# Kernel optimization log

Measured on AMD Instinct MI355X. Metric: run time of the kernel, lower is better.

The kernel has to match this reference:

```python
import jax, jax.numpy as jnp
import numpy as np
import math

B, S, N, D, H = 4, 64, 256, 512, 8
DEPTH = D // H

def setup_inputs() -> dict:
    key = jax.random.key(0)
    ks = jax.random.split(key, 9)
    scale = 1.0 / math.sqrt(D)
    return {
        "x": jax.random.normal(ks[0], (B, S, N, D), dtype=jnp.float32),
        "Wq": jax.random.normal(ks[1], (D, D), dtype=jnp.float32) * scale,
        "bq": jax.random.normal(ks[2], (D,), dtype=jnp.float32) * 0.01,
        "Wk": jax.random.normal(ks[3], (D, D), dtype=jnp.float32) * scale,
        "bk": jax.random.normal(ks[4], (D,), dtype=jnp.float32) * 0.01,
        "Wv": jax.random.normal(ks[5], (D, D), dtype=jnp.float32) * scale,
        "bv": jax.random.normal(ks[6], (D,), dtype=jnp.float32) * 0.01,
        "Wo": jax.random.normal(ks[7], (D, D), dtype=jnp.float32) * scale,
        "bo": jax.random.normal(ks[8], (D,), dtype=jnp.float32) * 0.01,
    }

def _split_heads(t):
    # (B, S, M, D) -> (B, H, S, M, depth); matches split_head.forward (4D path)
    # followed by the att_dim==2 permute(0, 2, 1, 3, 4) in cross_attention.
    b, s, m, _ = t.shape
    return t.reshape(b, s, m, H, DEPTH).transpose(0, 3, 1, 2, 4)

def reference(x, Wq, bq, Wk, bk, Wv, bv, Wo, bo):
    b, s, n, d = x.shape
    # att_dim == 2: query is the cls token along the joint/patch axis.
    q = _split_heads(x[:, :, 0:1, :] @ Wq + bq)   # (B, H, S, 1, depth)
    k = _split_heads(x @ Wk + bk)                  # (B, H, S, N, depth)
    v = _split_heads(x @ Wv + bv)                  # (B, H, S, N, depth)
    # scaled dot product attention (mask is None in cross_attention)
    logits = jnp.einsum('bhsqd,bhskd->bhsqk', q, k) / math.sqrt(DEPTH)
    attn = jax.nn.softmax(logits, axis=-1)         # (B, H, S, 1, N)
    ctx = jnp.einsum('bhsqk,bhskd->bhsqd', attn, v)  # (B, H, S, 1, depth)
    # permute(0, 2, 3, 1, 4) then reshape (B, S, 1, D)
    concat = ctx.transpose(0, 2, 3, 1, 4).reshape(b, s, 1, d)
    return concat @ Wo + bo
```

## Files before the change

### kernel.cpp

```cpp
#include <hip/hip_runtime.h>
#include <stdint.h>
#include <math.h>


#define NT 16

__global__ __launch_bounds__(1024, 4) void fused_kernel(
    const float* __restrict__ x,
    const float* __restrict__ Wq, const float* __restrict__ bq,
    const float* __restrict__ Wk,
    const float* __restrict__ Wv, const float* __restrict__ bv,
    const float* __restrict__ Wo, const float* __restrict__ bo,
    float* __restrict__ out) {
  const int bs = blockIdx.x;
  const int t = threadIdx.x;
  const int w = t >> 6, lane = t & 63;
  const float* xb = x + (long)bs * 131072;

  __shared__ float xt[2][NT * 512];
  __shared__ float r_s[4096];
  __shared__ float y_s[8 * 520];
  __shared__ float ypar[8][512];
  __shared__ float red_s[7][512];
  __shared__ float q_s[512];
  __shared__ float x0_s[512];
  __shared__ float ctx_s[512];
  __shared__ float pt_s[8][NT];
  __shared__ float f_s[8], s_s[8];

  if (t < 128) *(float4*)&x0_s[t * 4] = *(const float4*)&xb[t * 4];
  float4 st0 = *(const float4*)&xb[(long)t * 4];
  float4 st1 = *(const float4*)&xb[(long)(t + 1024) * 4];
  __syncthreads();

  {
    const int j4 = (t & 127) * 4;
    const int kq = t >> 7;
    float4 a = make_float4(0.f, 0.f, 0.f, 0.f);
    const float* wp = Wq + (long)(kq * 64) * 512 + j4;
    const float* ap = &x0_s[kq * 64];
#pragma unroll 8
    for (int k = 0; k < 64; ++k) {
      float4 wv = *(const float4*)&wp[(long)k * 512];
      float av = ap[k];
      a.x += av * wv.x; a.y += av * wv.y; a.z += av * wv.z; a.w += av * wv.w;
    }
    if (kq > 0) *(float4*)&red_s[kq - 1][j4] = a;
    __syncthreads();
    if (kq == 0) {
#pragma unroll
      for (int rr = 0; rr < 7; ++rr) {
        float4 b = *(const float4*)&red_s[rr][j4];
        a.x += b.x; a.y += b.y; a.z += b.z; a.w += b.w;
      }
      float4 bb = *(const float4*)&bq[j4];
      a.x += bb.x; a.y += bb.y; a.z += bb.z; a.w += bb.w;
      *(float4*)&q_s[j4] = a;
    }
  }
  __syncthreads();

  {
    const int d = t >> 1, hh = t & 1;
    const float* wrow = Wk + (long)d * 512 + hh * 256;
#pragma unroll
    for (int hi = 0; hi < 4; ++hi) {
      const int h = hh * 4 + hi;
      const float* qp = &q_s[h * 64];
      float racc = 0.f;
#pragma unroll
      for (int c4 = 0; c4 < 16; ++c4) {
        float4 wv = *(const float4*)&wrow[hi * 64 + c4 * 4];
        racc += qp[c4 * 4 + 0] * wv.x + qp[c4 * 4 + 1] * wv.y +
                qp[c4 * 4 + 2] * wv.z + qp[c4 * 4 + 3] * wv.w;
      }
      r_s[h * 512 + d] = racc;
    }
  }
  *(float4*)&xt[0][t * 4] = st0;
  *(float4*)&xt[0][(t + 1024) * 4] = st1;
  __syncthreads();

  const int hg = w & 1;
  const int rw = w >> 1;
  float rv[4][8];
#pragma unroll
  for (int hi = 0; hi < 4; ++hi) {
    const int h = hg * 4 + hi;
    float4 a = *(const float4*)&r_s[h * 512 + lane * 8];
    float4 b = *(const float4*)&r_s[h * 512 + lane * 8 + 4];
    rv[hi][0] = a.x; rv[hi][1] = a.y; rv[hi][2] = a.z; rv[hi][3] = a.w;
    rv[hi][4] = b.x; rv[hi][5] = b.y; rv[hi][6] = b.z; rv[hi][7] = b.w;
  }

  float accy[8] = {0.f, 0.f, 0.f, 0.f, 0.f, 0.f, 0.f, 0.f};
  float m_h = -INFINITY, s_h = 0.f;
  const int dcol = t & 511, halfn = t >> 9;

  for (int tile = 0; tile < 16; ++tile) {
    const int cur = tile & 1;
    float4 n0, n1;
    if (tile < 15) {
      const float* src = xb + (long)(tile + 1) * NT * 512;
      n0 = *(const float4*)&src[(long)t * 4];
      n1 = *(const float4*)&src[(long)(t + 1024) * 4];
    }

#pragma unroll
    for (int pass = 0; pass < 2; ++pass) {
      const int row = pass * 8 + rw;
      const float* xr = &xt[cur][row * 512 + lane * 8];
      float4 xa = *(const float4*)xr;
      float4 xb4 = *(const float4*)(xr + 4);
      float acc[4];
#pragma unroll
      for (int hi = 0; hi < 4; ++hi)
        acc[hi] = xa.x * rv[hi][0] + xa.y * rv[hi][1] + xa.z * rv[hi][2] + xa.w * rv[hi][3]
                + xb4.x * rv[hi][4] + xb4.y * rv[hi][5] + xb4.z * rv[hi][6] + xb4.w * rv[hi][7];
#pragma unroll
      for (int j = 0; j < 2; ++j) {
        float v = (lane & 2) ? acc[j] : acc[j + 2];
        float tt = __shfl_xor(v, 2);
        acc[j] = ((lane & 2) ? acc[j + 2] : acc[j]) + tt;
      }
      {
        float v = (lane & 1) ? acc[0] : acc[1];
        float tt = __shfl_xor(v, 1);
        acc[0] = ((lane & 1) ? acc[1] : acc[0]) + tt;
      }
      acc[0] += __shfl_xor(acc[0], 4);
      acc[0] += __shfl_xor(acc[0], 8);
      acc[0] += __shfl_xor(acc[0], 16);
      acc[0] += __shfl_xor(acc[0], 32);
      if (lane < 4) pt_s[hg * 4 + lane][row] = acc[0] * 0.125f;
    }
    __syncthreads();

    if (w < 8) {
      float l = (lane < 16) ? pt_s[w][lane] : -3.0e38f;
      float tm = l;
#pragma unroll
      for (int o = 8; o; o >>= 1) tm = fmaxf(tm, __shfl_xor(tm, o));
      float m_new = fmaxf(m_h, tm);
      float e = __expf(l - m_new);
      float ts = e;
#pragma unroll
      for (int o = 8; o; o >>= 1) ts += __shfl_xor(ts, o);
      float f = __expf(m_h - m_new);
      s_h = s_h * f + ts;
      m_h = m_new;
      if (lane == 0) f_s[w] = f;
      if (lane < 16) pt_s[w][lane] = e;
    }
    __syncthreads();

    if (tile < 15) {
      *(float4*)&xt[cur ^ 1][t * 4] = n0;
      *(float4*)&xt[cur ^ 1][(t + 1024) * 4] = n1;
    }

    {
#pragma unroll
      for (int h = 0; h < 8; ++h) accy[h] *= f_s[h];
#pragma unroll
      for (int n4 = 0; n4 < 2; ++n4) {
        const int nb = halfn * 8 + n4 * 4;
        float xv0 = xt[cur][(nb + 0) * 512 + dcol];
        float xv1 = xt[cur][(nb + 1) * 512 + dcol];
        float xv2 = xt[cur][(nb + 2) * 512 + dcol];
        float xv3 = xt[cur][(nb + 3) * 512 + dcol];
#pragma unroll
        for (int h = 0; h < 8; ++h) {
          float4 p4 = *(const float4*)&pt_s[h][nb];
          accy[h] += p4.x * xv0 + p4.y * xv1 + p4.z * xv2 + p4.w * xv3;
        }
      }
    }
    __syncthreads();
  }

  if (w < 8 && lane == 0) s_s[w] = s_h;
  __syncthreads();
  if (halfn == 1) {
#pragma unroll
    for (int h = 0; h < 8; ++h) ypar[h][dcol] = accy[h];
  }
  __syncthreads();
  if (halfn == 0) {
#pragma unroll
    for (int h = 0; h < 8; ++h)
      y_s[h * 520 + dcol] = (accy[h] + ypar[h][dcol]) * (1.f / s_s[h]);
  }
  __syncthreads();

  {
    const int o4 = (t & 127) * 4;
    const int kq = t >> 7;
    const int h0 = o4 >> 6;
    float4 a = make_float4(0.f, 0.f, 0.f, 0.f);
    const float* wp = Wv + (long)(kq * 64) * 512 + o4;
    const float* yp2 = &y_s[h0 * 520 + kq * 64];
#pragma unroll 8
    for (int k = 0; k < 64; ++k) {
      float4 wv = *(const float4*)&wp[(long)k * 512];
      float yv = yp2[k];
      a.x += yv * wv.x; a.y += yv * wv.y; a.z += yv * wv.z; a.w += yv * wv.w;
    }
    if (kq > 0) *(float4*)&red_s[kq - 1][o4] = a;
    __syncthreads();
    if (kq == 0) {
#pragma unroll
      for (int rr = 0; rr < 7; ++rr) {
        float4 b = *(const float4*)&red_s[rr][o4];
        a.x += b.x; a.y += b.y; a.z += b.z; a.w += b.w;
      }
      float4 bb = *(const float4*)&bv[o4];
      a.x += bb.x; a.y += bb.y; a.z += bb.z; a.w += bb.w;
      *(float4*)&ctx_s[o4] = a;
    }
  }
  __syncthreads();

  {
    const int j4 = (t & 127) * 4;
    const int kq = t >> 7;
    float4 a = make_float4(0.f, 0.f, 0.f, 0.f);
    const float* wp = Wo + (long)(kq * 64) * 512 + j4;
    const float* cp = &ctx_s[kq * 64];
#pragma unroll 8
    for (int k = 0; k < 64; ++k) {
      float4 wv = *(const float4*)&wp[(long)k * 512];
      float cv = cp[k];
      a.x += cv * wv.x; a.y += cv * wv.y; a.z += cv * wv.z; a.w += cv * wv.w;
    }
    if (kq > 0) *(float4*)&red_s[kq - 1][j4] = a;
    __syncthreads();
    if (kq == 0) {
#pragma unroll
      for (int rr = 0; rr < 7; ++rr) {
        float4 b = *(const float4*)&red_s[rr][j4];
        a.x += b.x; a.y += b.y; a.z += b.z; a.w += b.w;
      }
      float4 bb = *(const float4*)&bo[j4];
      a.x += bb.x; a.y += bb.y; a.z += bb.z; a.w += bb.w;
      *(float4*)&out[(long)bs * 512 + j4] = a;
    }
  }
}

extern "C" void kernel_launch(void* const* d_in, const int* in_sizes, int n_in,
                              void* d_out, int out_size, void* d_ws, size_t ws_size,
                              hipStream_t stream) {
  (void)in_sizes; (void)n_in; (void)out_size; (void)d_ws; (void)ws_size;
  const float* x  = (const float*)d_in[0];
  const float* Wq = (const float*)d_in[1];
  const float* bq = (const float*)d_in[2];
  const float* Wk = (const float*)d_in[3];
  const float* Wv = (const float*)d_in[5];
  const float* bv = (const float*)d_in[6];
  const float* Wo = (const float*)d_in[7];
  const float* bo = (const float*)d_in[8];
  float* out = (float*)d_out;

  fused_kernel<<<256, 1024, 0, stream>>>(x, Wq, bq, Wk, Wv, bv, Wo, bo, out);
}
```

Measured before the change: 280.3 us.

## Stream x tiles via direct global-to-LDS loads with triple buffering

Replaces the register-staged double buffer for x tiles with __builtin_amdgcn_global_load_lds into a three-slot LDS ring, prefetching two tiles ahead and gating each tile with s_waitcnt vmcnt plus raw s_barrier. The trailing per-tile __syncthreads is dropped, and the register round trip and LDS stores for staging are removed. Shared buffers are also aliased into one arena to hold the extra slot. This relies on hand-written waitcnt and barrier ordering; a wrong count or aliasing overlap would be a race.

```diff
diff --git a/kernel.cpp b/kernel.cpp
--- a/kernel.cpp
+++ b/kernel.cpp
@@ -4,6 +4,12 @@
 
 
 #define NT 16
+
+__device__ __forceinline__ void gload_lds16(const float* g, float* l) {
+  __builtin_amdgcn_global_load_lds(
+      (const __attribute__((address_space(1))) void*)g,
+      (__attribute__((address_space(3))) void*)l, 16, 0, 0);
+}
 
 __global__ __launch_bounds__(1024, 4) void fused_kernel(
     const float* __restrict__ x,
@@ -17,23 +23,24 @@
   const int w = t >> 6, lane = t & 63;
   const float* xb = x + (long)bs * 131072;
 
-  __shared__ float xt[2][NT * 512];
-  __shared__ float r_s[4096];
-  __shared__ float y_s[8 * 520];
-  __shared__ float ypar[8][512];
-  __shared__ float red_s[7][512];
-  __shared__ float q_s[512];
-  __shared__ float x0_s[512];
-  __shared__ float ctx_s[512];
-  __shared__ float pt_s[8][NT];
-  __shared__ float f_s[8], s_s[8];
+  __shared__ float arena[28672];
+  __shared__ float q_s[512], x0_s[512], ctx_s[512];
+  __shared__ float pt_s[8][NT], f_s[8], s_s[8];
+  float* const r_s = arena + 24576;
 
   if (t < 128) *(float4*)&x0_s[t * 4] = *(const float4*)&xb[t * 4];
-  float4 st0 = *(const float4*)&xb[(long)t * 4];
-  float4 st1 = *(const float4*)&xb[(long)(t + 1024) * 4];
-  __syncthreads();
-
-  {
+  {
+    float* b0 = arena;
+    float* b1 = arena + 8192;
+    gload_lds16(&xb[(long)t * 4],           b0 + w * 256);
+    gload_lds16(&xb[4096 + (long)t * 4],    b0 + 4096 + w * 256);
+    gload_lds16(&xb[8192 + (long)t * 4],    b1 + w * 256);
+    gload_lds16(&xb[12288 + (long)t * 4],   b1 + 4096 + w * 256);
+  }
+  __syncthreads();
+
+  {
+    float (*red_s)[512] = (float (*)[512])(arena + 16384);
     const int j4 = (t & 127) * 4;
     const int kq = t >> 7;
     float4 a = make_float4(0.f, 0.f, 0.f, 0.f);
@@ -77,8 +84,6 @@
       r_s[h * 512 + d] = racc;
     }
   }
-  *(float4*)&xt[0][t * 4] = st0;
-  *(float4*)&xt[0][(t + 1024) * 4] = st1;
   __syncthreads();
 
   const int hg = w & 1;
@@ -98,18 +103,29 @@
   const int dcol = t & 511, halfn = t >> 9;
 
   for (int tile = 0; tile < 16; ++tile) {
-    const int cur = tile & 1;
-    float4 n0, n1;
+    const int cur = tile % 3;
+    const float* xt = arena + cur * 8192;
+
     if (tile < 15) {
-      const float* src = xb + (long)(tile + 1) * NT * 512;
-      n0 = *(const float4*)&src[(long)t * 4];
-      n1 = *(const float4*)&src[(long)(t + 1024) * 4];
+      asm volatile("s_waitcnt vmcnt(2)" ::: "memory");
+    } else {
+      asm volatile("s_waitcnt vmcnt(0)" ::: "memory");
+    }
+    __builtin_amdgcn_sched_barrier(0);
+    __builtin_amdgcn_s_barrier();
+    __builtin_amdgcn_sched_barrier(0);
+
+    if (tile + 2 < 16) {
+      const float* src = xb + (long)(tile + 2) * 8192;
+      float* dst = arena + ((tile + 2) % 3) * 8192;
+      gload_lds16(&src[(long)t * 4],        dst + w * 256);
+      gload_lds16(&src[4096 + (long)t * 4], dst + 4096 + w * 256);
     }
 
 #pragma unroll
     for (int pass = 0; pass < 2; ++pass) {
       const int row = pass * 8 + rw;
-      const float* xr = &xt[cur][row * 512 + lane * 8];
+      const float* xr = &xt[row * 512 + lane * 8];
       float4 xa = *(const float4*)xr;
       float4 xb4 = *(const float4*)(xr + 4);
       float acc[4];
@@ -134,7 +150,10 @@
       acc[0] += __shfl_xor(acc[0], 32);
       if (lane < 4) pt_s[hg * 4 + lane][row] = acc[0] * 0.125f;
     }
-    __syncthreads();
+    asm volatile("s_waitcnt lgkmcnt(0)" ::: "memory");
+    __builtin_amdgcn_sched_barrier(0);
+    __builtin_amdgcn_s_barrier();
+    __builtin_amdgcn_sched_barrier(0);
 
     if (w < 8) {
       float l = (lane < 16) ? pt_s[w][lane] : -3.0e38f;
@@ -152,12 +171,10 @@
       if (lane == 0) f_s[w] = f;
       if (lane < 16) pt_s[w][lane] = e;
     }
-    __syncthreads();
-
-    if (tile < 15) {
-      *(float4*)&xt[cur ^ 1][t * 4] = n0;
-      *(float4*)&xt[cur ^ 1][(t + 1024) * 4] = n1;
-    }
+    asm volatile("s_waitcnt lgkmcnt(0)" ::: "memory");
+    __builtin_amdgcn_sched_barrier(0);
+    __builtin_amdgcn_s_barrier();
+    __builtin_amdgcn_sched_barrier(0);
 
     {
 #pragma unroll
@@ -165,10 +182,10 @@
 #pragma unroll
       for (int n4 = 0; n4 < 2; ++n4) {
         const int nb = halfn * 8 + n4 * 4;
-        float xv0 = xt[cur][(nb + 0) * 512 + dcol];
-        float xv1 = xt[cur][(nb + 1) * 512 + dcol];
-        float xv2 = xt[cur][(nb + 2) * 512 + dcol];
-        float xv3 = xt[cur][(nb + 3) * 512 + dcol];
+        float xv0 = xt[(nb + 0) * 512 + dcol];
+        float xv1 = xt[(nb + 1) * 512 + dcol];
+        float xv2 = xt[(nb + 2) * 512 + dcol];
+        float xv3 = xt[(nb + 3) * 512 + dcol];
 #pragma unroll
         for (int h = 0; h < 8; ++h) {
           float4 p4 = *(const float4*)&pt_s[h][nb];
@@ -176,30 +193,32 @@
         }
       }
     }
-    __syncthreads();
   }
 
   if (w < 8 && lane == 0) s_s[w] = s_h;
   __syncthreads();
+  float* ypar = arena;
+  float* y_sp = arena + 4096;
   if (halfn == 1) {
 #pragma unroll
-    for (int h = 0; h < 8; ++h) ypar[h][dcol] = accy[h];
+    for (int h = 0; h < 8; ++h) ypar[h * 512 + dcol] = accy[h];
   }
   __syncthreads();
   if (halfn == 0) {
 #pragma unroll
     for (int h = 0; h < 8; ++h)
-      y_s[h * 520 + dcol] = (accy[h] + ypar[h][dcol]) * (1.f / s_s[h]);
-  }
-  __syncthreads();
-
-  {
+      y_sp[h * 520 + dcol] = (accy[h] + ypar[h * 512 + dcol]) * (1.f / s_s[h]);
+  }
+  __syncthreads();
+
+  {
+    float (*red_s)[512] = (float (*)[512])(arena + 16384);
     const int o4 = (t & 127) * 4;
     const int kq = t >> 7;
     const int h0 = o4 >> 6;
     float4 a = make_float4(0.f, 0.f, 0.f, 0.f);
     const float* wp = Wv + (long)(kq * 64) * 512 + o4;
-    const float* yp2 = &y_s[h0 * 520 + kq * 64];
+    const float* yp2 = &y_sp[h0 * 520 + kq * 64];
 #pragma unroll 8
     for (int k = 0; k < 64; ++k) {
       float4 wv = *(const float4*)&wp[(long)k * 512];
@@ -222,6 +241,7 @@
   __syncthreads();
 
   {
+    float (*red_s)[512] = (float (*)[512])(arena + 16384);
     const int j4 = (t & 127) * 4;
     const int kq = t >> 7;
     float4 a = make_float4(0.f, 0.f, 0.f, 0.f);
```

After: 306.9 us. 9.5% more time.

## Drop shared-memory x tile staging; use register prefetch and global reloads

Applied to the files above, without the earlier changes.

Removes the double-buffered shared-memory x tile. Each thread now keeps the x values it needs for the logit dot products in registers, prefetched one tile ahead, and reads x directly from global memory (expected to hit L2/cache) for the weighted-sum accumulation. pt_s and f_s are double-buffered so the trailing barrier per tile can be dropped. This cuts LDS footprint and one sync per tile, at the cost of a second global read of each x element and extra register pressure.

```diff
diff --git a/kernel.cpp b/kernel.cpp
--- a/kernel.cpp
+++ b/kernel.cpp
@@ -17,20 +17,23 @@
   const int w = t >> 6, lane = t & 63;
   const float* xb = x + (long)bs * 131072;
 
-  __shared__ float xt[2][NT * 512];
+  __shared__ float q_s[512], x0_s[512], ctx_s[512];
   __shared__ float r_s[4096];
-  __shared__ float y_s[8 * 520];
+  __shared__ float red_s[7][512];
   __shared__ float ypar[8][512];
-  __shared__ float red_s[7][512];
-  __shared__ float q_s[512];
-  __shared__ float x0_s[512];
-  __shared__ float ctx_s[512];
-  __shared__ float pt_s[8][NT];
-  __shared__ float f_s[8], s_s[8];
+  __shared__ float y_sp[8][520];
+  __shared__ float pt_s[2][8][NT];
+  __shared__ float f_s[2][8];
+  __shared__ float s_s[8];
+
+  const int hg = w & 1;
+  const int rw = w >> 1;
 
   if (t < 128) *(float4*)&x0_s[t * 4] = *(const float4*)&xb[t * 4];
-  float4 st0 = *(const float4*)&xb[(long)t * 4];
-  float4 st1 = *(const float4*)&xb[(long)(t + 1024) * 4];
+  float4 c00 = *(const float4*)&xb[(long)rw * 512 + lane * 8];
+  float4 c01 = *(const float4*)&xb[(long)rw * 512 + lane * 8 + 4];
+  float4 c10 = *(const float4*)&xb[(long)(8 + rw) * 512 + lane * 8];
+  float4 c11 = *(const float4*)&xb[(long)(8 + rw) * 512 + lane * 8 + 4];
   __syncthreads();
 
   {
@@ -77,12 +80,8 @@
       r_s[h * 512 + d] = racc;
     }
   }
-  *(float4*)&xt[0][t * 4] = st0;
-  *(float4*)&xt[0][(t + 1024) * 4] = st1;
-  __syncthreads();
-
-  const int hg = w & 1;
-  const int rw = w >> 1;
+  __syncthreads();
+
   float rv[4][8];
 #pragma unroll
   for (int hi = 0; hi < 4; ++hi) {
@@ -98,25 +97,14 @@
   const int dcol = t & 511, halfn = t >> 9;
 
   for (int tile = 0; tile < 16; ++tile) {
-    const int cur = tile & 1;
-    float4 n0, n1;
-    if (tile < 15) {
-      const float* src = xb + (long)(tile + 1) * NT * 512;
-      n0 = *(const float4*)&src[(long)t * 4];
-      n1 = *(const float4*)&src[(long)(t + 1024) * 4];
-    }
-
-#pragma unroll
-    for (int pass = 0; pass < 2; ++pass) {
-      const int row = pass * 8 + rw;
-      const float* xr = &xt[cur][row * 512 + lane * 8];
-      float4 xa = *(const float4*)xr;
-      float4 xb4 = *(const float4*)(xr + 4);
+    const int b = tile & 1;
+
+    {
       float acc[4];
 #pragma unroll
       for (int hi = 0; hi < 4; ++hi)
-        acc[hi] = xa.x * rv[hi][0] + xa.y * rv[hi][1] + xa.z * rv[hi][2] + xa.w * rv[hi][3]
-                + xb4.x * rv[hi][4] + xb4.y * rv[hi][5] + xb4.z * rv[hi][6] + xb4.w * rv[hi][7];
+        acc[hi] = c00.x * rv[hi][0] + c00.y * rv[hi][1] + c00.z * rv[hi][2] + c00.w * rv[hi][3]
+                + c01.x * rv[hi][4] + c01.y * rv[hi][5] + c01.z * rv[hi][6] + c01.w * rv[hi][7];
 #pragma unroll
       for (int j = 0; j < 2; ++j) {
         float v = (lane & 2) ? acc[j] : acc[j + 2];
@@ -132,12 +120,32 @@
       acc[0] += __shfl_xor(acc[0], 8);
       acc[0] += __shfl_xor(acc[0], 16);
       acc[0] += __shfl_xor(acc[0], 32);
-      if (lane < 4) pt_s[hg * 4 + lane][row] = acc[0] * 0.125f;
+      if (lane < 4) pt_s[b][hg * 4 + lane][rw] = acc[0] * 0.125f;
+#pragma unroll
+      for (int hi = 0; hi < 4; ++hi)
+        acc[hi] = c10.x * rv[hi][0] + c10.y * rv[hi][1] + c10.z * rv[hi][2] + c10.w * rv[hi][3]
+                + c11.x * rv[hi][4] + c11.y * rv[hi][5] + c11.z * rv[hi][6] + c11.w * rv[hi][7];
+#pragma unroll
+      for (int j = 0; j < 2; ++j) {
+        float v = (lane & 2) ? acc[j] : acc[j + 2];
+        float tt = __shfl_xor(v, 2);
+        acc[j] = ((lane & 2) ? acc[j + 2] : acc[j]) + tt;
+      }
+      {
+        float v = (lane & 1) ? acc[0] : acc[1];
+        float tt = __shfl_xor(v, 1);
+        acc[0] = ((lane & 1) ? acc[1] : acc[0]) + tt;
+      }
+      acc[0] += __shfl_xor(acc[0], 4);
+      acc[0] += __shfl_xor(acc[0], 8);
+      acc[0] += __shfl_xor(acc[0], 16);
+      acc[0] += __shfl_xor(acc[0], 32);
+      if (lane < 4) pt_s[b][hg * 4 + lane][8 + rw] = acc[0] * 0.125f;
     }
     __syncthreads();
 
     if (w < 8) {
-      float l = (lane < 16) ? pt_s[w][lane] : -3.0e38f;
+      float l = (lane < 16) ? pt_s[b][w][lane] : -3.0e38f;
       float tm = l;
 #pragma unroll
       for (int o = 8; o; o >>= 1) tm = fmaxf(tm, __shfl_xor(tm, o));
@@ -149,34 +157,39 @@
       float f = __expf(m_h - m_new);
       s_h = s_h * f + ts;
       m_h = m_new;
-      if (lane == 0) f_s[w] = f;
-      if (lane < 16) pt_s[w][lane] = e;
-    }
-    __syncthreads();
-
+      if (lane == 0) f_s[b][w] = f;
+      if (lane < 16) pt_s[b][w][lane] = e;
+    }
+    __syncthreads();
+
+    float4 n00, n01, n10, n11;
     if (tile < 15) {
-      *(float4*)&xt[cur ^ 1][t * 4] = n0;
-      *(float4*)&xt[cur ^ 1][(t + 1024) * 4] = n1;
+      const float* nx = xb + (long)(tile + 1) * 8192;
+      n00 = *(const float4*)&nx[(long)rw * 512 + lane * 8];
+      n01 = *(const float4*)&nx[(long)rw * 512 + lane * 8 + 4];
+      n10 = *(const float4*)&nx[(long)(8 + rw) * 512 + lane * 8];
+      n11 = *(const float4*)&nx[(long)(8 + rw) * 512 + lane * 8 + 4];
     }
 
     {
 #pragma unroll
-      for (int h = 0; h < 8; ++h) accy[h] *= f_s[h];
+      for (int h = 0; h < 8; ++h) accy[h] *= f_s[b][h];
+      const float* xg = xb + ((long)tile * 16 + halfn * 8) * 512 + dcol;
 #pragma unroll
       for (int n4 = 0; n4 < 2; ++n4) {
         const int nb = halfn * 8 + n4 * 4;
-        float xv0 = xt[cur][(nb + 0) * 512 + dcol];
-        float xv1 = xt[cur][(nb + 1) * 512 + dcol];
-        float xv2 = xt[cur][(nb + 2) * 512 + dcol];
-        float xv3 = xt[cur][(nb + 3) * 512 + dcol];
+        float xv0 = xg[(long)(n4 * 4 + 0) * 512];
+        float xv1 = xg[(long)(n4 * 4 + 1) * 512];
+        float xv2 = xg[(long)(n4 * 4 + 2) * 512];
+        float xv3 = xg[(long)(n4 * 4 + 3) * 512];
 #pragma unroll
         for (int h = 0; h < 8; ++h) {
-          float4 p4 = *(const float4*)&pt_s[h][nb];
+          float4 p4 = *(const float4*)&pt_s[b][h][nb];
           accy[h] += p4.x * xv0 + p4.y * xv1 + p4.z * xv2 + p4.w * xv3;
         }
       }
     }
-    __syncthreads();
+    if (tile < 15) { c00 = n00; c01 = n01; c10 = n10; c11 = n11; }
   }
 
   if (w < 8 && lane == 0) s_s[w] = s_h;
@@ -189,7 +202,7 @@
   if (halfn == 0) {
 #pragma unroll
     for (int h = 0; h < 8; ++h)
-      y_s[h * 520 + dcol] = (accy[h] + ypar[h][dcol]) * (1.f / s_s[h]);
+      y_sp[h][dcol] = (accy[h] + ypar[h][dcol]) * (1.f / s_s[h]);
   }
   __syncthreads();
 
@@ -199,7 +212,7 @@
     const int h0 = o4 >> 6;
     float4 a = make_float4(0.f, 0.f, 0.f, 0.f);
     const float* wp = Wv + (long)(kq * 64) * 512 + o4;
-    const float* yp2 = &y_s[h0 * 520 + kq * 64];
+    const float* yp2 = &y_sp[h0][kq * 64];
 #pragma unroll 8
     for (int k = 0; k < 64; ++k) {
       float4 wv = *(const float4*)&wp[(long)k * 512];
```

Result: slower. 296.4 us (+5.8%).
